# Kernel tuning notes

Hardware: AMD Instinct MI355X
Metric: run time of the kernel (lower is better)

## Reference

```python
import jax, jax.numpy as jnp
import numpy as np

EPS = 1e-12

def l2norm(x, axis):
    # torch.nn.functional.normalize: x / max(||x||_2, eps)
    n = jnp.sqrt(jnp.sum(x * x, axis=axis, keepdims=True))
    return x / jnp.maximum(n, EPS)

def setup_inputs() -> dict:
    key = jax.random.key(0)
    k1, k2, k3, k4 = jax.random.split(key, 4)
    B, Cf, H, W = 128, 1024, 16, 16
    n_att, dv = 312, 300
    img = jax.random.normal(k1, (B, Cf, H, W), dtype=jnp.float32)
    # V is initialized from row-normalized w2v embeddings in the module
    V = l2norm(jax.random.normal(k2, (n_att, dv), dtype=jnp.float32), axis=1)
    W1 = jax.random.normal(k3, (dv, Cf), dtype=jnp.float32)
    W2 = jax.random.normal(k4, (dv, Cf), dtype=jnp.float32)
    return {"img": img, "V": V, "W1": W1, "W2": W2}

def reference(img, V, W1, W2):
    vv = l2norm(V, axis=1)                               # [i, v]
    B, Cf, H, Wd = img.shape
    av = l2norm(img.reshape(B, Cf, H * Wd), axis=1)      # [b, f, r]
    Q = vv @ W1                                          # [i, f]
    A = jnp.einsum('if,bfr->bir', Q, av)                 # attention logits
    A = jax.nn.softmax(A, axis=-1)
    F_p = jnp.einsum('bir,bfr->bif', A, av)              # attended features
    Pred_att = jnp.einsum('if,bif->bi', vv @ W2, F_p)
    return Pred_att
```

## Files before the change

### kernel.cpp

```cpp
#include <hip/hip_runtime.h>
#include <math.h>

#define NB   128
#define CF   1024
#define RR   256
#define NA   312
#define DV   300
#define MT   640
#define NKC  32
#define NQ   160

typedef _Float16 half8  __attribute__((ext_vector_type(8)));
typedef _Float16 half4  __attribute__((ext_vector_type(4)));
typedef float float16v  __attribute__((ext_vector_type(16)));
typedef float float4v   __attribute__((ext_vector_type(4)));

__device__ __forceinline__ void gll16(const void* g, void* l) {
    __builtin_amdgcn_global_load_lds(
        (const __attribute__((address_space(1))) void*)g,
        (__attribute__((address_space(3))) void*)l, 16, 0, 0);
}

__launch_bounds__(256, 6)
__global__ void k_pq(const float* __restrict__ img, float* __restrict__ ssq32,
                     _Float16* __restrict__ avT,
                     const float* __restrict__ V, const float* __restrict__ W1,
                     const float* __restrict__ W2, _Float16* __restrict__ Qb) {
    int lin = blockIdx.x;
    int t = threadIdx.x;
    if (lin >= NQ) {
        int m  = lin - NQ;
        int kc = m & 31;
        int b  = m >> 5;
        int kk8 = t & 3;
        int rq  = t >> 2;
        const float* src = img + ((size_t)b * CF + kc * 32 + kk8 * 8) * RR + rq * 4;
        float4v v[8];
        #pragma unroll
        for (int j = 0; j < 8; ++j) v[j] = *(const float4v*)(src + (size_t)j * RR);
        float ss0 = 0.f, ss1 = 0.f, ss2 = 0.f, ss3 = 0.f;
        #pragma unroll
        for (int j = 0; j < 8; ++j) {
            ss0 += v[j][0] * v[j][0]; ss1 += v[j][1] * v[j][1];
            ss2 += v[j][2] * v[j][2]; ss3 += v[j][3] * v[j][3];
        }
        _Float16* dst = avT + ((size_t)(b * NKC + kc) * RR + rq * 4) * 32 + kk8 * 8;
        #pragma unroll
        for (int s = 0; s < 4; ++s) {
            half8 o;
            #pragma unroll
            for (int j = 0; j < 8; ++j) o[j] = (_Float16)v[j][s];
            *(half8*)(dst + (size_t)s * 32) = o;
        }
        ss0 += __shfl_xor(ss0, 1, 64); ss0 += __shfl_xor(ss0, 2, 64);
        ss1 += __shfl_xor(ss1, 1, 64); ss1 += __shfl_xor(ss1, 2, 64);
        ss2 += __shfl_xor(ss2, 1, 64); ss2 += __shfl_xor(ss2, 2, 64);
        ss3 += __shfl_xor(ss3, 1, 64); ss3 += __shfl_xor(ss3, 2, 64);
        if (kk8 == 0) {
            float4v sv; sv[0] = ss0; sv[1] = ss1; sv[2] = ss2; sv[3] = ss3;
            *(float4v*)(ssq32 + ((size_t)b * NKC + kc) * RR + rq * 4) = sv;
        }
    } else {
        int ib = lin;
        bool isQ2 = ib >= 80;
        int i0l = (ib - (isQ2 ? 80 : 0)) * 4;
        __shared__ float inv4[4];
        float acc[4][4];
        #pragma unroll
        for (int ii = 0; ii < 4; ++ii)
            #pragma unroll
            for (int j = 0; j < 4; ++j) acc[ii][j] = 0.f;
        if (i0l < NA) {
            int row = t >> 6, l64 = t & 63;
            float s = 0.f;
            for (int v = l64; v < DV; v += 64) { float x = V[(i0l + row) * DV + v]; s += x * x; }
            #pragma unroll
            for (int o = 32; o; o >>= 1) s += __shfl_xor(s, o, 64);
            if (l64 == 0) inv4[row] = 1.f / fmaxf(sqrtf(s), 1e-12f);
            __syncthreads();
            const float* W  = isQ2 ? W2 : W1;
            const float* Vb = V + (size_t)i0l * DV;
            for (int v = 0; v < DV; v += 2) {
                float4v w0 = *(const float4v*)(W + (size_t)v * CF + t * 4);
                float4v w1 = *(const float4v*)(W + (size_t)(v + 1) * CF + t * 4);
                #pragma unroll
                for (int ii = 0; ii < 4; ++ii) {
                    float a0 = Vb[(size_t)ii * DV + v];
                    float a1 = Vb[(size_t)ii * DV + v + 1];
                    #pragma unroll
                    for (int j = 0; j < 4; ++j) acc[ii][j] += a0 * w0[j] + a1 * w1[j];
                }
            }
            #pragma unroll
            for (int ii = 0; ii < 4; ++ii)
                #pragma unroll
                for (int j = 0; j < 4; ++j) acc[ii][j] *= inv4[ii];
        }
        int fg = t >> 3;
        int fo = (t & 7) * 4;
        int q12 = isQ2 ? 1 : 0;
        #pragma unroll
        for (int ii = 0; ii < 4; ++ii) {
            half4 h;
            #pragma unroll
            for (int j = 0; j < 4; ++j) h[j] = (_Float16)acc[ii][j];
            *(half4*)&Qb[((size_t)fg * MT + (2 * (i0l + ii) + q12)) * 32 + fo] = h;
        }
    }
}

extern __shared__ char smem[];
__launch_bounds__(512, 2)
__global__ void k_gemm(const _Float16* __restrict__ Qb, const _Float16* __restrict__ avT,
                       const float* __restrict__ ssq32, float* __restrict__ out) {
    int lin = blockIdx.x;
    int xcd = lin & 7;
    int u   = lin >> 3;
    int b   = xcd + 8 * (u & 15);
    int t2h = u >> 4;

    int tid  = threadIdx.x;
    int lane = tid & 63;
    int w    = tid >> 6;
    int wm   = w >> 2;
    int wn   = w & 3;
    int nl   = lane & 31;
    int kh   = lane >> 5;

    int c1 = 512 + tid;
    int a_s0 = (tid % 320) * 64 + (tid / 320) * 16;
    int a_s1 = (c1 % 320) * 64 + (c1 / 320) * 16;
    int a_s2 = ((tid & 255) + 64) * 64 + 3 * 16;
    int a_d0 = tid * 16;
    int a_d1 = a_d0 + 8192;
    int a_d2 = 16384 + (tid & 255) * 16;
    int b_s0 = (tid & 255) * 64 + (tid >> 8) * 16;

    const char* Abase_g = (const char*)Qb;
    const char* Bbase_g = (const char*)avT + ((size_t)b * NKC) * RR * 64;

    float16v acc[5][2];
    #pragma unroll
    for (int i = 0; i < 5; ++i)
        #pragma unroll
        for (int j = 0; j < 2; ++j)
            #pragma unroll
            for (int gi = 0; gi < 16; ++gi) acc[i][j][gi] = 0.f;

    char* p0 = smem;
    char* p1 = smem + 36864;
    char* p2 = smem + 73728;

    #define STAGE(kc_, buf) do {                                                   \
        int kcl = (kc_) < NKC ? (kc_) : (NKC - 1);                                 \
        const char* aS = Abase_g + ((size_t)kcl * MT + (size_t)t2h * 320) * 64;    \
        const char* bS = Bbase_g + (size_t)kcl * RR * 64;                          \
        char* ab = (buf); char* bb = (buf) + 20480;                                \
        gll16(aS + a_s0, ab + a_d0);                                               \
        gll16(aS + a_s1, ab + a_d1);                                               \
        gll16(aS + a_s2, ab + a_d2);                                               \
        gll16(bS + b_s0,      bb + tid * 16);                                      \
        gll16(bS + b_s0 + 32, bb + tid * 16 + 8192);                               \
    } while (0)

    #define COMPUTE(buf) do {                                                      \
        const char* Al = (buf); const char* Bl = (buf) + 20480;                    \
        _Pragma("unroll")                                                          \
        for (int ks = 0; ks < 2; ++ks) {                                           \
            int kb = ks * 2 + kh;                                                  \
            half8 bf0 = *(const half8*)(Bl + ((size_t)kb * 256 + wn * 64 + nl) * 16);      \
            half8 bf1 = *(const half8*)(Bl + ((size_t)kb * 256 + wn * 64 + 32 + nl) * 16); \
            _Pragma("unroll")                                                      \
            for (int mt = 0; mt < 5; ++mt) {                                       \
                half8 af = *(const half8*)(Al + ((size_t)kb * 320 + wm * 160 + mt * 32 + nl) * 16); \
                acc[mt][0] = __builtin_amdgcn_mfma_f32_32x32x16_f16(af, bf0, acc[mt][0], 0, 0, 0);  \
                acc[mt][1] = __builtin_amdgcn_mfma_f32_32x32x16_f16(af, bf1, acc[mt][1], 0, 0, 0);  \
            }                                                                      \
        }                                                                          \
    } while (0)

    STAGE(0, p0);
    __builtin_amdgcn_sched_barrier(0);
    STAGE(1, p1);
    asm volatile("s_waitcnt vmcnt(5)" ::: "memory");
    __builtin_amdgcn_s_barrier();
    __builtin_amdgcn_sched_barrier(0);

    #pragma unroll 1
    for (int kc = 0; kc < NKC; ++kc) {
        STAGE(kc + 2, p2);
        asm volatile("s_waitcnt vmcnt(5)" ::: "memory");
        __builtin_amdgcn_sched_barrier(0);
        COMPUTE(p0);
        __builtin_amdgcn_sched_barrier(0);
        __builtin_amdgcn_s_barrier();
        char* tmp = p0; p0 = p1; p1 = p2; p2 = tmp;
    }
    asm volatile("s_waitcnt vmcnt(0)" ::: "memory");
    __builtin_amdgcn_s_barrier();
    __builtin_amdgcn_sched_barrier(0);
    #undef STAGE
    #undef COMPUTE

    float* mred = (float*)smem;
    float* mg   = (float*)(smem + 2560);
    float* sred = (float*)(smem + 3200);
    float* dred = (float*)(smem + 5760);

    const float* sq = ssq32 + (size_t)b * NKC * RR;
    int c0 = wn * 64 + nl;
    float q0 = 0.f, q1 = 0.f;
    #pragma unroll
    for (int kc = 0; kc < NKC; ++kc) {
        q0 += sq[(size_t)kc * RR + c0];
        q1 += sq[(size_t)kc * RR + 32 + c0];
    }
    float iv0 = 1.f / fmaxf(sqrtf(q0), 1e-12f);
    float iv1 = 1.f / fmaxf(sqrtf(q1), 1e-12f);
    #pragma unroll
    for (int mt = 0; mt < 5; ++mt)
        #pragma unroll
        for (int gi = 0; gi < 16; ++gi) {
            acc[mt][0][gi] *= iv0;
            acc[mt][1][gi] *= iv1;
        }

    #pragma unroll
    for (int mt = 0; mt < 5; ++mt) {
        #pragma unroll
        for (int e = 0; e < 8; ++e) {
            int g = 2 * e;
            float mx = fmaxf(acc[mt][0][g], acc[mt][1][g]);
            #pragma unroll
            for (int off = 1; off <= 16; off <<= 1)
                mx = fmaxf(mx, __shfl_xor(mx, off, 64));
            if (nl == 0) {
                int row = (g & 3) + 8 * (g >> 2) + 4 * kh;
                mred[wn * 160 + wm * 80 + mt * 16 + (row >> 1)] = mx;
            }
        }
    }
    __syncthreads();
    if (tid < 160)
        mg[tid] = fmaxf(fmaxf(mred[tid], mred[160 + tid]),
                        fmaxf(mred[320 + tid], mred[480 + tid]));
    __syncthreads();

    #pragma unroll
    for (int mt = 0; mt < 5; ++mt) {
        #pragma unroll
        for (int e = 0; e < 8; ++e) {
            int g = 2 * e;
            int row = (g & 3) + 8 * (g >> 2) + 4 * kh;
            int Pl = wm * 80 + mt * 16 + (row >> 1);
            float m = mg[Pl];
            float e0 = __expf(acc[mt][0][g] - m);
            float e1 = __expf(acc[mt][1][g] - m);
            float s = e0 + e1;
            float d = e0 * acc[mt][0][g + 1] + e1 * acc[mt][1][g + 1];
            #pragma unroll
            for (int off = 1; off <= 16; off <<= 1) {
                s += __shfl_xor(s, off, 64);
                d += __shfl_xor(d, off, 64);
            }
            if (nl == 0) {
                sred[wn * 160 + Pl] = s;
                dred[wn * 160 + Pl] = d;
            }
        }
    }
    __syncthreads();
    if (tid < 160) {
        float s = sred[tid] + sred[160 + tid] + sred[320 + tid] + sred[480 + tid];
        float d = dred[tid] + dred[160 + tid] + dred[320 + tid] + dred[480 + tid];
        int ig = t2h * 160 + tid;
        if (ig < NA) out[b * NA + ig] = d / s;
    }
}

extern "C" void kernel_launch(void* const* d_in, const int* in_sizes, int n_in,
                              void* d_out, int out_size, void* d_ws, size_t ws_size,
                              hipStream_t stream) {
    const float* img = (const float*)d_in[0];
    const float* V   = (const float*)d_in[1];
    const float* W1  = (const float*)d_in[2];
    const float* W2  = (const float*)d_in[3];
    float* out = (float*)d_out;

    char* ws = (char*)d_ws;
    size_t off = 0;
    float*    ssq32 = (float*)(ws + off);    off += (size_t)NB * NKC * RR * 4;
    _Float16* avT   = (_Float16*)(ws + off); off += (size_t)NB * CF * RR * 2;
    _Float16* Qb    = (_Float16*)(ws + off); off += (size_t)NKC * MT * 32 * 2;

    static bool attr_done = false;
    if (!attr_done) {
        hipFuncSetAttribute((const void*)k_gemm,
                            hipFuncAttributeMaxDynamicSharedMemorySize, 110592);
        attr_done = true;
    }

    k_pq<<<dim3(NQ + NB * NKC), 256, 0, stream>>>(img, ssq32, avT, V, W1, W2, Qb);
    k_gemm<<<dim3(256), 512, 110592, stream>>>(Qb, avT, ssq32, out);
}
```

Before: 283.2 us.

## Split prep and Q kernels; stage img tile via LDS direct loads

```diff
diff --git a/kernel.cpp b/kernel.cpp
--- a/kernel.cpp
+++ b/kernel.cpp
@@ -21,91 +21,89 @@
         (__attribute__((address_space(3))) void*)l, 16, 0, 0);
 }
 
-__launch_bounds__(256, 6)
-__global__ void k_pq(const float* __restrict__ img, float* __restrict__ ssq32,
-                     _Float16* __restrict__ avT,
-                     const float* __restrict__ V, const float* __restrict__ W1,
-                     const float* __restrict__ W2, _Float16* __restrict__ Qb) {
-    int lin = blockIdx.x;
-    int t = threadIdx.x;
-    if (lin >= NQ) {
-        int m  = lin - NQ;
-        int kc = m & 31;
-        int b  = m >> 5;
-        int kk8 = t & 3;
-        int rq  = t >> 2;
-        const float* src = img + ((size_t)b * CF + kc * 32 + kk8 * 8) * RR + rq * 4;
-        float4v v[8];
-        #pragma unroll
-        for (int j = 0; j < 8; ++j) v[j] = *(const float4v*)(src + (size_t)j * RR);
-        float ss0 = 0.f, ss1 = 0.f, ss2 = 0.f, ss3 = 0.f;
-        #pragma unroll
-        for (int j = 0; j < 8; ++j) {
-            ss0 += v[j][0] * v[j][0]; ss1 += v[j][1] * v[j][1];
-            ss2 += v[j][2] * v[j][2]; ss3 += v[j][3] * v[j][3];
+__launch_bounds__(256, 4)
+__global__ void k_prep(const float* __restrict__ img, float* __restrict__ ssq32,
+                       _Float16* __restrict__ avT) {
+    int m  = blockIdx.x;
+    int kc = m & 31;
+    int b  = m >> 5;
+    int t  = threadIdx.x;
+    __shared__ __align__(16) float tile[32][256];
+
+    const char* src = (const char*)(img + ((size_t)b * CF + kc * 32) * RR);
+    #pragma unroll
+    for (int i = 0; i < 8; ++i)
+        gll16(src + (size_t)i * 4096 + (size_t)t * 16,
+              (char*)tile + i * 4096 + t * 16);
+    asm volatile("s_waitcnt vmcnt(0)" ::: "memory");
+    __syncthreads();
+
+    float v[32];
+    #pragma unroll
+    for (int f = 0; f < 32; ++f) v[f] = tile[f][t];
+    float ss = 0.f;
+    #pragma unroll
+    for (int f = 0; f < 32; ++f) ss += v[f] * v[f];
+
+    _Float16* dst = avT + ((size_t)(b * NKC + kc) * RR + t) * 32;
+    #pragma unroll
+    for (int s = 0; s < 4; ++s) {
+        half8 o;
+        #pragma unroll
+        for (int j = 0; j < 8; ++j) o[j] = (_Float16)v[s * 8 + j];
+        *(half8*)(dst + s * 8) = o;
+    }
+    ssq32[(size_t)(b * NKC + kc) * RR + t] = ss;
+}
+
+__launch_bounds__(256, 4)
+__global__ void k_q(const float* __restrict__ V, const float* __restrict__ W1,
+                    const float* __restrict__ W2, _Float16* __restrict__ Qb) {
+    int ib = blockIdx.x;
+    int t  = threadIdx.x;
+    bool isQ2 = ib >= 80;
+    int i0l = (ib - (isQ2 ? 80 : 0)) * 4;
+    __shared__ float inv4[4];
+    float acc[4][4];
+    #pragma unroll
+    for (int ii = 0; ii < 4; ++ii)
+        #pragma unroll
+        for (int j = 0; j < 4; ++j) acc[ii][j] = 0.f;
+    if (i0l < NA) {
+        int row = t >> 6, l64 = t & 63;
+        float s = 0.f;
+        for (int v = l64; v < DV; v += 64) { float x = V[(i0l + row) * DV + v]; s += x * x; }
+        #pragma unroll
+        for (int o = 32; o; o >>= 1) s += __shfl_xor(s, o, 64);
+        if (l64 == 0) inv4[row] = 1.f / fmaxf(sqrtf(s), 1e-12f);
+        __syncthreads();
+        const float* W  = isQ2 ? W2 : W1;
+        const float* Vb = V + (size_t)i0l * DV;
+        for (int v = 0; v < DV; v += 2) {
+            float4v w0 = *(const float4v*)(W + (size_t)v * CF + t * 4);
+            float4v w1 = *(const float4v*)(W + (size_t)(v + 1) * CF + t * 4);
+            #pragma unroll
+            for (int ii = 0; ii < 4; ++ii) {
+                float a0 = Vb[(size_t)ii * DV + v];
+                float a1 = Vb[(size_t)ii * DV + v + 1];
+                #pragma unroll
+                for (int j = 0; j < 4; ++j) acc[ii][j] += a0 * w0[j] + a1 * w1[j];
+            }
         }
-        _Float16* dst = avT + ((size_t)(b * NKC + kc) * RR + rq * 4) * 32 + kk8 * 8;
-        #pragma unroll
-        for (int s = 0; s < 4; ++s) {
-            half8 o;
-            #pragma unroll
-            for (int j = 0; j < 8; ++j) o[j] = (_Float16)v[j][s];
-            *(half8*)(dst + (size_t)s * 32) = o;
-        }
-        ss0 += __shfl_xor(ss0, 1, 64); ss0 += __shfl_xor(ss0, 2, 64);
-        ss1 += __shfl_xor(ss1, 1, 64); ss1 += __shfl_xor(ss1, 2, 64);
-        ss2 += __shfl_xor(ss2, 1, 64); ss2 += __shfl_xor(ss2, 2, 64);
-        ss3 += __shfl_xor(ss3, 1, 64); ss3 += __shfl_xor(ss3, 2, 64);
-        if (kk8 == 0) {
-            float4v sv; sv[0] = ss0; sv[1] = ss1; sv[2] = ss2; sv[3] = ss3;
-            *(float4v*)(ssq32 + ((size_t)b * NKC + kc) * RR + rq * 4) = sv;
-        }
-    } else {
-        int ib = lin;
-        bool isQ2 = ib >= 80;
-        int i0l = (ib - (isQ2 ? 80 : 0)) * 4;
-        __shared__ float inv4[4];
-        float acc[4][4];
         #pragma unroll
         for (int ii = 0; ii < 4; ++ii)
             #pragma unroll
-            for (int j = 0; j < 4; ++j) acc[ii][j] = 0.f;
-        if (i0l < NA) {
-            int row = t >> 6, l64 = t & 63;
-            float s = 0.f;
-            for (int v = l64; v < DV; v += 64) { float x = V[(i0l + row) * DV + v]; s += x * x; }
-            #pragma unroll
-            for (int o = 32; o; o >>= 1) s += __shfl_xor(s, o, 64);
-            if (l64 == 0) inv4[row] = 1.f / fmaxf(sqrtf(s), 1e-12f);
-            __syncthreads();
-            const float* W  = isQ2 ? W2 : W1;
-            const float* Vb = V + (size_t)i0l * DV;
-            for (int v = 0; v < DV; v += 2) {
-                float4v w0 = *(const float4v*)(W + (size_t)v * CF + t * 4);
-                float4v w1 = *(const float4v*)(W + (size_t)(v + 1) * CF + t * 4);
-                #pragma unroll
-                for (int ii = 0; ii < 4; ++ii) {
-                    float a0 = Vb[(size_t)ii * DV + v];
-                    float a1 = Vb[(size_t)ii * DV + v + 1];
-                    #pragma unroll
-                    for (int j = 0; j < 4; ++j) acc[ii][j] += a0 * w0[j] + a1 * w1[j];
-                }
-            }
-            #pragma unroll
-            for (int ii = 0; ii < 4; ++ii)
-                #pragma unroll
-                for (int j = 0; j < 4; ++j) acc[ii][j] *= inv4[ii];
-        }
-        int fg = t >> 3;
-        int fo = (t & 7) * 4;
-        int q12 = isQ2 ? 1 : 0;
-        #pragma unroll
-        for (int ii = 0; ii < 4; ++ii) {
-            half4 h;
-            #pragma unroll
-            for (int j = 0; j < 4; ++j) h[j] = (_Float16)acc[ii][j];
-            *(half4*)&Qb[((size_t)fg * MT + (2 * (i0l + ii) + q12)) * 32 + fo] = h;
-        }
+            for (int j = 0; j < 4; ++j) acc[ii][j] *= inv4[ii];
+    }
+    int fg = t >> 3;
+    int fo = (t & 7) * 4;
+    int q12 = isQ2 ? 1 : 0;
+    #pragma unroll
+    for (int ii = 0; ii < 4; ++ii) {
+        half4 h;
+        #pragma unroll
+        for (int j = 0; j < 4; ++j) h[j] = (_Float16)acc[ii][j];
+        *(half4*)&Qb[((size_t)fg * MT + (2 * (i0l + ii) + q12)) * 32 + fo] = h;
     }
 }
 
@@ -300,6 +298,7 @@
         attr_done = true;
     }
 
-    k_pq<<<dim3(NQ + NB * NKC), 256, 0, stream>>>(img, ssq32, avT, V, W1, W2, Qb);
+    k_prep<<<dim3(NB * NKC), 256, 0, stream>>>(img, ssq32, avT);
+    k_q<<<dim3(NQ), 256, 0, stream>>>(V, W1, W2, Qb);
     k_gemm<<<dim3(256), 512, 110592, stream>>>(Qb, avT, ssq32, out);
 }
```

Measured after the change: 298.5 us. 1.05x slower.
